# Kernel tuning notes

Hardware: AMD Instinct MI355X
Metric: run time of the kernel (lower is better)

Reference implementation:

```python
import jax, jax.numpy as jnp
import numpy as np

N, M, D = 100000, 5000, 2

def setup_inputs() -> dict:
    key = jax.random.key(0)
    k1, k2, k3 = jax.random.split(key, 3)
    euclidean_data = jax.random.normal(k1, (N, D), dtype=jnp.float32)
    maze_points = jax.random.normal(k2, (M, D), dtype=jnp.float32)
    ts_proj = jax.random.uniform(k3, (M,), dtype=jnp.float32)
    return {"euclidean_data": euclidean_data, "maze_points": maze_points, "ts_proj": ts_proj}

def reference(euclidean_data, maze_points, ts_proj):
    # squared distance matrix [N, M], reduced via argmin (1-NN)
    diff = euclidean_data[:, None, :] - maze_points[None, :, :]   # [N, M, D]
    dist2 = jnp.sum(jnp.square(diff), axis=-1)                    # [N, M]
    best = jnp.argmin(dist2, axis=1)                              # [N]
    projected_pos = maze_points[best]                             # [N, D]
    linear_pos = ts_proj[best]                                    # [N]
    return (projected_pos, linear_pos)
```

## Files before the change

### kernel.cpp

```cpp
#include <hip/hip_runtime.h>

#define N_Q  100000
#define N_M  5000
#define G    64
#define NC   (G * G)
#define RMAX 4
#define CS_OFF_B   64
#define SORT_OFF_B (CS_OFF_B + 16400)
#define OVF_OFF_B  (SORT_OFF_B + N_M * 16)
#define WS_NEED    (OVF_OFF_B + N_Q * 4)

__global__ __launch_bounds__(1024) void build_grid(
    const float* __restrict__ maze, const float* __restrict__ ts,
    float* __restrict__ ws)
{
    __shared__ float red[1024];
    __shared__ int   part[1024];
    __shared__ int   cnt[NC];
    const int t = threadIdx.x;
    if (t == 0) ((int*)ws)[8] = 0;

    float mnx = 1e30f, mxx = -1e30f, mny = 1e30f, mxy = -1e30f;
    for (int i = t; i < N_M; i += 1024) {
        const float x = maze[2 * i], y = maze[2 * i + 1];
        mnx = fminf(mnx, x); mxx = fmaxf(mxx, x);
        mny = fminf(mny, y); mxy = fmaxf(mxy, y);
    }
    auto reduce = [&](float v, bool domin) -> float {
        red[t] = v; __syncthreads();
        for (int s = 512; s > 0; s >>= 1) {
            if (t < s) {
                const float o = red[t + s];
                red[t] = domin ? fminf(red[t], o) : fmaxf(red[t], o);
            }
            __syncthreads();
        }
        const float r = red[0]; __syncthreads(); return r;
    };
    mnx = reduce(mnx, true);  mxx = reduce(mxx, false);
    mny = reduce(mny, true);  mxy = reduce(mxy, false);

    float cwx = (mxx - mnx) * (1.0f / G) * (1.0f + 1e-5f);
    float cwy = (mxy - mny) * (1.0f / G) * (1.0f + 1e-5f);
    if (!(cwx > 0.0f)) cwx = 1.0f;
    if (!(cwy > 0.0f)) cwy = 1.0f;
    const float ivx = 1.0f / cwx, ivy = 1.0f / cwy;
    if (t == 0) {
        ws[0] = mnx; ws[1] = mny; ws[2] = cwx;
        ws[3] = cwy; ws[4] = ivx; ws[5] = ivy;
    }

    for (int i = t; i < NC; i += 1024) cnt[i] = 0;
    __syncthreads();
    for (int i = t; i < N_M; i += 1024) {
        const float x = maze[2 * i], y = maze[2 * i + 1];
        const int cx = min(G - 1, max(0, (int)((x - mnx) * ivx)));
        const int cy = min(G - 1, max(0, (int)((y - mny) * ivy)));
        atomicAdd(&cnt[cy * G + cx], 1);
    }
    __syncthreads();

    int* cs = (int*)((char*)ws + CS_OFF_B);
    const int base = t * 4;
    int loc[4], sum = 0;
    #pragma unroll
    for (int j = 0; j < 4; ++j) { loc[j] = sum; sum += cnt[base + j]; }
    part[t] = sum; __syncthreads();
    for (int s = 1; s < 1024; s <<= 1) {
        const int v = (t >= s) ? part[t - s] : 0;
        __syncthreads();
        part[t] += v;
        __syncthreads();
    }
    const int excl = part[t] - sum;
    #pragma unroll
    for (int j = 0; j < 4; ++j) cs[base + j] = excl + loc[j];
    if (t == 0) cs[NC] = N_M;
    __syncthreads();
    #pragma unroll
    for (int j = 0; j < 4; ++j) cnt[base + j] = excl + loc[j];
    __syncthreads();

    float4* sorted = (float4*)((char*)ws + SORT_OFF_B);
    for (int i = t; i < N_M; i += 1024) {
        const float x = maze[2 * i], y = maze[2 * i + 1];
        const int cx = min(G - 1, max(0, (int)((x - mnx) * ivx)));
        const int cy = min(G - 1, max(0, (int)((y - mny) * ivy)));
        const int pos = atomicAdd(&cnt[cy * G + cx], 1);
        float4 e; e.x = x; e.y = y; e.z = ts[i]; e.w = __int_as_float(i);
        sorted[pos] = e;
    }
}

__global__ __launch_bounds__(256) void grid_query(
    const float* __restrict__ q, float* __restrict__ ws,
    float* __restrict__ out)
{
    const int qi = blockIdx.x * 256 + threadIdx.x;
    if (qi >= N_Q) return;

    const float mnx = ws[0], mny = ws[1], cwx = ws[2];
    const float cwy = ws[3], ivx = ws[4], ivy = ws[5];
    const int*    cs     = (const int*)((const char*)ws + CS_OFF_B);
    const float4* sorted = (const float4*)((const char*)ws + SORT_OFF_B);

    const float2 Q = ((const float2*)q)[qi];
    const float qx = Q.x, qy = Q.y;
    const int cx = min(G - 1, max(0, (int)((qx - mnx) * ivx)));
    const int cy = min(G - 1, max(0, (int)((qy - mny) * ivy)));

    float bd2 = 3.4e38f;
    int bidx = 0x7fffffff, bsp = 0;

    auto scan_pts = [&](int s, int e) {
        for (int p = s; p < e; ++p) {
            const float4 c = sorted[p];
            const float dx = __fsub_rn(qx, c.x);
            const float dy = __fsub_rn(qy, c.y);
            const float d2 = __fadd_rn(__fmul_rn(dx, dx), __fmul_rn(dy, dy));
            const int idx = __float_as_int(c.w);
            if (d2 < bd2 || (d2 == bd2 && idx < bidx)) { bd2 = d2; bidx = idx; bsp = p; }
        }
    };
    auto scan_row = [&](int rowbase, int xa, int xb) {
        int prev = cs[rowbase + xa];
        for (int x = xa; x <= xb; ++x) {
            const int nxt = cs[rowbase + x + 1];
            scan_pts(prev, nxt);
            prev = nxt;
        }
    };

    bool resolved = false;
    for (int r = 0; r <= RMAX; ++r) {
        const int x0 = max(0, cx - r), x1 = min(G - 1, cx + r);
        if (r == 0) {
            scan_row(cy * G, cx, cx);
        } else {
            if (cy - r >= 0)     scan_row((cy - r) * G, x0, x1);
            if (cy + r <= G - 1) scan_row((cy + r) * G, x0, x1);
            const int yy0 = max(0, cy - r + 1), yy1 = min(G - 1, cy + r - 1);
            if (cx - r >= 0)     for (int y = yy0; y <= yy1; ++y) { const int c0 = y * G + cx - r; scan_pts(cs[c0], cs[c0 + 1]); }
            if (cx + r <= G - 1) for (int y = yy0; y <= yy1; ++y) { const int c0 = y * G + cx + r; scan_pts(cs[c0], cs[c0 + 1]); }
        }
        const float Xlo = mnx + (float)(cx - r) * cwx;
        const float Xhi = mnx + (float)(cx + r + 1) * cwx;
        const float Ylo = mny + (float)(cy - r) * cwy;
        const float Yhi = mny + (float)(cy + r + 1) * cwy;
        float lb = fminf(fminf(qx - Xlo, Xhi - qx), fminf(qy - Ylo, Yhi - qy));
        lb = lb * 0.9999f - 1e-6f;
        if (lb > 0.0f && lb * lb > bd2) { resolved = true; break; }
    }

    if (resolved) {
        const float4 bw = sorted[bsp];
        out[2 * qi]       = bw.x;
        out[2 * qi + 1]   = bw.y;
        out[2 * N_Q + qi] = bw.z;
    } else {
        int* ovfc = (int*)ws + 8;
        const int pos = atomicAdd(ovfc, 1);
        ((int*)((char*)ws + OVF_OFF_B))[pos] = qi;
    }
}

__global__ __launch_bounds__(256) void brute_overflow(
    const float* __restrict__ q, const float* __restrict__ maze,
    const float* __restrict__ ts, const float* __restrict__ ws,
    float* __restrict__ out)
{
    const int cnt = ((const int*)ws)[8];
    const int* ovl = (const int*)((const char*)ws + OVF_OFF_B);
    const int wave  = (blockIdx.x * 256 + threadIdx.x) >> 6;
    const int lane  = threadIdx.x & 63;
    const int nwave = gridDim.x * 4;

    for (int w = wave; w < cnt; w += nwave) {
        const int qi = ovl[w];
        const float qx = q[2 * qi], qy = q[2 * qi + 1];
        float bd2 = 3.4e38f; int bidx = 0x7fffffff;
        for (int p = lane; p < N_M; p += 64) {
            const float2 c = ((const float2*)maze)[p];
            const float dx = __fsub_rn(qx, c.x);
            const float dy = __fsub_rn(qy, c.y);
            const float d2 = __fadd_rn(__fmul_rn(dx, dx), __fmul_rn(dy, dy));
            if (d2 < bd2 || (d2 == bd2 && p < bidx)) { bd2 = d2; bidx = p; }
        }
        #pragma unroll
        for (int s = 1; s < 64; s <<= 1) {
            const float ob = __shfl_xor(bd2, s);
            const int   oi = __shfl_xor(bidx, s);
            if (ob < bd2 || (ob == bd2 && oi < bidx)) { bd2 = ob; bidx = oi; }
        }
        if (lane == 0) {
            out[2 * qi]       = maze[2 * bidx];
            out[2 * qi + 1]   = maze[2 * bidx + 1];
            out[2 * N_Q + qi] = ts[bidx];
        }
    }
}

#define CW   4
#define CHK  1264
#define NPAD (CW * CHK)
#define FB_WS_BYTES (NPAD * 2 * 4)

typedef float v2f __attribute__((ext_vector_type(2)));
typedef float v8f __attribute__((ext_vector_type(8)));

__global__ void setup_soa(const float* __restrict__ maze, float* __restrict__ ws) {
    const int i = blockIdx.x * 256 + threadIdx.x;
    if (i >= NPAD) return;
    const int c = i / CHK, k = i - c * CHK;
    float x = 1e30f, y = 1e30f;
    const int g = c * 1250 + k;
    if (k < 1250) { x = -maze[2 * g]; y = -maze[2 * g + 1]; }
    ws[i] = x;
    ws[NPAD + i] = y;
}

#define LDX0(D) asm volatile("s_load_dwordx8 %0, %1, 0x0"    : "=s"(D) : "s"(xb))
#define LDX1(D) asm volatile("s_load_dwordx8 %0, %1, 0x20"   : "=s"(D) : "s"(xb))
#define LDY0(D) asm volatile("s_load_dwordx8 %0, %1, 0x4f00" : "=s"(D) : "s"(xb))
#define LDY1(D) asm volatile("s_load_dwordx8 %0, %1, 0x4f20" : "=s"(D) : "s"(xb))
#define WAIT4(a,b,c,d) asm volatile("s_waitcnt lgkmcnt(0)" : "+s"(a), "+s"(b), "+s"(c), "+s"(d))

#define PSTEP(X8, Y8, J) do {                                                 \
    v2f px_ = __builtin_shufflevector(X8, X8, 2*(J), 2*(J)+1);                \
    v2f py_ = __builtin_shufflevector(Y8, Y8, 2*(J), 2*(J)+1);                \
    v2f dx_, dy_;                                                             \
    asm("v_pk_add_f32 %0, %1, %2" : "=v"(dx_) : "s"(px_), "v"(qxx));          \
    asm("v_pk_add_f32 %0, %1, %2" : "=v"(dy_) : "s"(py_), "v"(qyy));          \
    asm("v_pk_mul_f32 %0, %0, %0" : "+v"(dx_));                               \
    asm("v_pk_mul_f32 %0, %0, %0" : "+v"(dy_));                               \
    asm("v_pk_add_f32 %0, %0, %1" : "+v"(dx_) : "v"(dy_));                    \
    float a_ = dx_.x, b_ = dx_.y;                                             \
    asm("v_min3_f32 %0, %1, %2, %0" : "+v"(bm) : "v"(a_), "v"(b_));           \
} while (0)

#define COMP(X0, X1, Y0, Y1, B) do {                                          \
    PSTEP(X0, Y0, 0); PSTEP(X0, Y0, 1); PSTEP(X0, Y0, 2); PSTEP(X0, Y0, 3);   \
    PSTEP(X1, Y1, 0); PSTEP(X1, Y1, 1); PSTEP(X1, Y1, 2); PSTEP(X1, Y1, 3);   \
    bb = (bm < prev) ? (B) : bb; prev = bm;                                   \
} while (0)

__global__ __launch_bounds__(256) void nn_scan(
    const float* __restrict__ q, const float* __restrict__ maze,
    const float* __restrict__ ts, const float* __restrict__ ws,
    float* __restrict__ out)
{
    __shared__ float sval[CW][64];
    __shared__ int   sidx[CW][64];
    const int lane = threadIdx.x & 63;
    const int wv   = __builtin_amdgcn_readfirstlane((int)(threadIdx.x >> 6));
    const int qi   = blockIdx.x * 64 + lane;
    const int qc   = qi < N_Q ? qi : N_Q - 1;
    const float2 Q = ((const float2*)q)[qc];
    const v2f qxx = { Q.x, Q.x };
    const v2f qyy = { Q.y, Q.y };
    unsigned long long xb = (unsigned long long)(const void*)(ws + (size_t)wv * CHK);
    v8f ax0, ax1, ay0, ay1, bx0, bx1, by0, by1;
    LDX0(ax0); LDX1(ax1); LDY0(ay0); LDY1(ay1); xb += 64;
    float bm = 3.4e38f, prev = 3.4e38f;
    int bb = 0;
    #pragma unroll 1
    for (int k = 0; k < 39; ++k) {
        WAIT4(ax0, ax1, ay0, ay1);
        LDX0(bx0); LDX1(bx1); LDY0(by0); LDY1(by1); xb += 64;
        COMP(ax0, ax1, ay0, ay1, 2 * k);
        WAIT4(bx0, bx1, by0, by1);
        LDX0(ax0); LDX1(ax1); LDY0(ay0); LDY1(ay1); xb += 64;
        COMP(bx0, bx1, by0, by1, 2 * k + 1);
    }
    WAIT4(ax0, ax1, ay0, ay1);
    COMP(ax0, ax1, ay0, ay1, 78);
    int fk = 0x7fffffff;
    {
        const float* xs = ws + (size_t)wv * CHK + (size_t)bb * 16;
        #pragma unroll
        for (int j = 0; j < 16; ++j) {
            const float dx = __fadd_rn(Q.x, xs[j]);
            const float dy = __fadd_rn(Q.y, xs[j + NPAD]);
            const float d2 = __fadd_rn(__fmul_rn(dx, dx), __fmul_rn(dy, dy));
            if (d2 == bm) fk = min(fk, bb * 16 + j);
        }
    }
    const int kloc = fk < 1250 ? fk : 1249;
    sval[wv][lane] = bm;
    sidx[wv][lane] = wv * 1250 + kloc;
    __syncthreads();
    if (wv == 0 && qi < N_Q) {
        float bv = sval[0][lane];
        int   bg = sidx[0][lane];
        #pragma unroll
        for (int c = 1; c < CW; ++c) {
            const float v = sval[c][lane];
            const int   g = sidx[c][lane];
            if (v < bv || (v == bv && g < bg)) { bv = v; bg = g; }
        }
        const float2 bp = ((const float2*)maze)[bg];
        out[2 * qi]       = bp.x;
        out[2 * qi + 1]   = bp.y;
        out[2 * N_Q + qi] = ts[bg];
    }
}

extern "C" void kernel_launch(void* const* d_in, const int* in_sizes, int n_in,
                              void* d_out, int out_size, void* d_ws, size_t ws_size,
                              hipStream_t stream) {
    const float* q    = (const float*)d_in[0];
    const float* maze = (const float*)d_in[1];
    const float* ts   = (const float*)d_in[2];
    float* out = (float*)d_out;

    if (ws_size >= (size_t)WS_NEED) {
        build_grid<<<1, 1024, 0, stream>>>(maze, ts, (float*)d_ws);
        grid_query<<<(N_Q + 255) / 256, 256, 0, stream>>>(q, (float*)d_ws, out);
        brute_overflow<<<256, 256, 0, stream>>>(q, maze, ts, (const float*)d_ws, out);
    } else {
        setup_soa<<<(NPAD + 255) / 256, 256, 0, stream>>>(maze, (float*)d_ws);
        nn_scan<<<(N_Q + 63) / 64, 256, 0, stream>>>(q, maze, ts,
                                                     (const float*)d_ws, out);
    }
}
```

Baseline: 76.81 us.

## Fuse overflow brute force into grid query and shrink grid search to two rings

The overflow kernel and its atomic queue are removed. Unresolved queries are now brute-forced inside the query kernel, with the whole wave cooperating on each unresolved lane found via ballot. The query scans the 3x3 neighborhood as three contiguous row ranges with 4-wide unrolled loads, then ring 2 only if needed, and falls back to brute force after that. The grid build uses 256 threads with wave-shuffle reductions instead of shared-memory tree reductions, saving a launch and barriers at the cost of divergence when some lanes need the fallback.

Measured after the change: 91.53 us. 1.19x slower.

```diff
diff --git a/kernel.cpp b/kernel.cpp
--- a/kernel.cpp
+++ b/kernel.cpp
@@ -4,55 +4,48 @@
 #define N_M  5000
 #define G    64
 #define NC   (G * G)
-#define RMAX 4
 #define CS_OFF_B   64
 #define SORT_OFF_B (CS_OFF_B + 16400)
-#define OVF_OFF_B  (SORT_OFF_B + N_M * 16)
-#define WS_NEED    (OVF_OFF_B + N_Q * 4)
-
-__global__ __launch_bounds__(1024) void build_grid(
+#define WS_NEED    (SORT_OFF_B + N_M * 16)
+
+__global__ __launch_bounds__(256) void build_grid(
     const float* __restrict__ maze, const float* __restrict__ ts,
     float* __restrict__ ws)
 {
-    __shared__ float red[1024];
-    __shared__ int   part[1024];
     __shared__ int   cnt[NC];
-    const int t = threadIdx.x;
-    if (t == 0) ((int*)ws)[8] = 0;
+    __shared__ int   part[256];
+    __shared__ float wred[4][4];
+    const int t = threadIdx.x, lane = t & 63, wv = t >> 6;
 
     float mnx = 1e30f, mxx = -1e30f, mny = 1e30f, mxy = -1e30f;
-    for (int i = t; i < N_M; i += 1024) {
+    for (int i = t; i < N_M; i += 256) {
         const float x = maze[2 * i], y = maze[2 * i + 1];
         mnx = fminf(mnx, x); mxx = fmaxf(mxx, x);
         mny = fminf(mny, y); mxy = fmaxf(mxy, y);
     }
-    auto reduce = [&](float v, bool domin) -> float {
-        red[t] = v; __syncthreads();
-        for (int s = 512; s > 0; s >>= 1) {
-            if (t < s) {
-                const float o = red[t + s];
-                red[t] = domin ? fminf(red[t], o) : fmaxf(red[t], o);
-            }
-            __syncthreads();
-        }
-        const float r = red[0]; __syncthreads(); return r;
-    };
-    mnx = reduce(mnx, true);  mxx = reduce(mxx, false);
-    mny = reduce(mny, true);  mxy = reduce(mxy, false);
+    #pragma unroll
+    for (int s = 1; s < 64; s <<= 1) {
+        mnx = fminf(mnx, __shfl_xor(mnx, s));
+        mxx = fmaxf(mxx, __shfl_xor(mxx, s));
+        mny = fminf(mny, __shfl_xor(mny, s));
+        mxy = fmaxf(mxy, __shfl_xor(mxy, s));
+    }
+    if (lane == 0) { wred[wv][0] = mnx; wred[wv][1] = mxx; wred[wv][2] = mny; wred[wv][3] = mxy; }
+    for (int i = t; i < NC; i += 256) cnt[i] = 0;
+    __syncthreads();
+    mnx = fminf(fminf(wred[0][0], wred[1][0]), fminf(wred[2][0], wred[3][0]));
+    mxx = fmaxf(fmaxf(wred[0][1], wred[1][1]), fmaxf(wred[2][1], wred[3][1]));
+    mny = fminf(fminf(wred[0][2], wred[1][2]), fminf(wred[2][2], wred[3][2]));
+    mxy = fmaxf(fmaxf(wred[0][3], wred[1][3]), fmaxf(wred[2][3], wred[3][3]));
 
     float cwx = (mxx - mnx) * (1.0f / G) * (1.0f + 1e-5f);
     float cwy = (mxy - mny) * (1.0f / G) * (1.0f + 1e-5f);
     if (!(cwx > 0.0f)) cwx = 1.0f;
     if (!(cwy > 0.0f)) cwy = 1.0f;
     const float ivx = 1.0f / cwx, ivy = 1.0f / cwy;
-    if (t == 0) {
-        ws[0] = mnx; ws[1] = mny; ws[2] = cwx;
-        ws[3] = cwy; ws[4] = ivx; ws[5] = ivy;
-    }
-
-    for (int i = t; i < NC; i += 1024) cnt[i] = 0;
-    __syncthreads();
-    for (int i = t; i < N_M; i += 1024) {
+    if (t == 0) { ws[0] = mnx; ws[1] = mny; ws[2] = cwx; ws[3] = cwy; ws[4] = ivx; ws[5] = ivy; }
+
+    for (int i = t; i < N_M; i += 256) {
         const float x = maze[2 * i], y = maze[2 * i + 1];
         const int cx = min(G - 1, max(0, (int)((x - mnx) * ivx)));
         const int cy = min(G - 1, max(0, (int)((y - mny) * ivy)));
@@ -61,12 +54,12 @@
     __syncthreads();
 
     int* cs = (int*)((char*)ws + CS_OFF_B);
-    const int base = t * 4;
-    int loc[4], sum = 0;
+    const int base = t * 16;
+    int loc[16], sum = 0;
     #pragma unroll
-    for (int j = 0; j < 4; ++j) { loc[j] = sum; sum += cnt[base + j]; }
+    for (int j = 0; j < 16; ++j) { loc[j] = sum; sum += cnt[base + j]; }
     part[t] = sum; __syncthreads();
-    for (int s = 1; s < 1024; s <<= 1) {
+    for (int s = 1; s < 256; s <<= 1) {
         const int v = (t >= s) ? part[t - s] : 0;
         __syncthreads();
         part[t] += v;
@@ -74,15 +67,15 @@
     }
     const int excl = part[t] - sum;
     #pragma unroll
-    for (int j = 0; j < 4; ++j) cs[base + j] = excl + loc[j];
+    for (int j = 0; j < 16; ++j) cs[base + j] = excl + loc[j];
     if (t == 0) cs[NC] = N_M;
     __syncthreads();
     #pragma unroll
-    for (int j = 0; j < 4; ++j) cnt[base + j] = excl + loc[j];
+    for (int j = 0; j < 16; ++j) cnt[base + j] = excl + loc[j];
     __syncthreads();
 
     float4* sorted = (float4*)((char*)ws + SORT_OFF_B);
-    for (int i = t; i < N_M; i += 1024) {
+    for (int i = t; i < N_M; i += 256) {
         const float x = maze[2 * i], y = maze[2 * i + 1];
         const int cx = min(G - 1, max(0, (int)((x - mnx) * ivx)));
         const int cy = min(G - 1, max(0, (int)((y - mny) * ivy)));
@@ -92,118 +85,109 @@
     }
 }
 
-__global__ __launch_bounds__(256) void grid_query(
-    const float* __restrict__ q, float* __restrict__ ws,
+__global__ __launch_bounds__(64) void grid_query(
+    const float* __restrict__ q, const float* __restrict__ maze,
+    const float* __restrict__ ts, const float* __restrict__ ws,
     float* __restrict__ out)
 {
-    const int qi = blockIdx.x * 256 + threadIdx.x;
-    if (qi >= N_Q) return;
+    const int lane = threadIdx.x;
+    const int qi = blockIdx.x * 64 + lane;
+    const int qc = qi < N_Q ? qi : N_Q - 1;
 
     const float mnx = ws[0], mny = ws[1], cwx = ws[2];
     const float cwy = ws[3], ivx = ws[4], ivy = ws[5];
     const int*    cs     = (const int*)((const char*)ws + CS_OFF_B);
     const float4* sorted = (const float4*)((const char*)ws + SORT_OFF_B);
 
-    const float2 Q = ((const float2*)q)[qi];
+    const float2 Q = ((const float2*)q)[qc];
     const float qx = Q.x, qy = Q.y;
     const int cx = min(G - 1, max(0, (int)((qx - mnx) * ivx)));
     const int cy = min(G - 1, max(0, (int)((qy - mny) * ivy)));
 
     float bd2 = 3.4e38f;
-    int bidx = 0x7fffffff, bsp = 0;
-
-    auto scan_pts = [&](int s, int e) {
-        for (int p = s; p < e; ++p) {
-            const float4 c = sorted[p];
-            const float dx = __fsub_rn(qx, c.x);
-            const float dy = __fsub_rn(qy, c.y);
-            const float d2 = __fadd_rn(__fmul_rn(dx, dx), __fmul_rn(dy, dy));
-            const int idx = __float_as_int(c.w);
-            if (d2 < bd2 || (d2 == bd2 && idx < bidx)) { bd2 = d2; bidx = idx; bsp = p; }
-        }
+    int bidx = 0x7fffffff;
+
+    auto cand = [&](const float4 c) {
+        const float dx = __fsub_rn(qx, c.x);
+        const float dy = __fsub_rn(qy, c.y);
+        const float d2 = __fadd_rn(__fmul_rn(dx, dx), __fmul_rn(dy, dy));
+        const int idx = __float_as_int(c.w);
+        if (d2 < bd2 || (d2 == bd2 && idx < bidx)) { bd2 = d2; bidx = idx; }
     };
-    auto scan_row = [&](int rowbase, int xa, int xb) {
-        int prev = cs[rowbase + xa];
-        for (int x = xa; x <= xb; ++x) {
-            const int nxt = cs[rowbase + x + 1];
-            scan_pts(prev, nxt);
-            prev = nxt;
+    auto scan4 = [&](int s, int e) {
+        for (int p = s; p < e; p += 4) {
+            const float4 c0 = sorted[p];
+            const float4 c1 = sorted[p + 1 < e ? p + 1 : p];
+            const float4 c2 = sorted[p + 2 < e ? p + 2 : p];
+            const float4 c3 = sorted[p + 3 < e ? p + 3 : p];
+            cand(c0); cand(c1); cand(c2); cand(c3);
         }
     };
-
-    bool resolved = false;
-    for (int r = 0; r <= RMAX; ++r) {
-        const int x0 = max(0, cx - r), x1 = min(G - 1, cx + r);
-        if (r == 0) {
-            scan_row(cy * G, cx, cx);
-        } else {
-            if (cy - r >= 0)     scan_row((cy - r) * G, x0, x1);
-            if (cy + r <= G - 1) scan_row((cy + r) * G, x0, x1);
-            const int yy0 = max(0, cy - r + 1), yy1 = min(G - 1, cy + r - 1);
-            if (cx - r >= 0)     for (int y = yy0; y <= yy1; ++y) { const int c0 = y * G + cx - r; scan_pts(cs[c0], cs[c0 + 1]); }
-            if (cx + r <= G - 1) for (int y = yy0; y <= yy1; ++y) { const int c0 = y * G + cx + r; scan_pts(cs[c0], cs[c0 + 1]); }
-        }
+    auto bound_ok = [&](int r) -> bool {
         const float Xlo = mnx + (float)(cx - r) * cwx;
         const float Xhi = mnx + (float)(cx + r + 1) * cwx;
         const float Ylo = mny + (float)(cy - r) * cwy;
         const float Yhi = mny + (float)(cy + r + 1) * cwy;
         float lb = fminf(fminf(qx - Xlo, Xhi - qx), fminf(qy - Ylo, Yhi - qy));
         lb = lb * 0.9999f - 1e-6f;
-        if (lb > 0.0f && lb * lb > bd2) { resolved = true; break; }
-    }
-
-    if (resolved) {
-        const float4 bw = sorted[bsp];
-        out[2 * qi]       = bw.x;
-        out[2 * qi + 1]   = bw.y;
-        out[2 * N_Q + qi] = bw.z;
-    } else {
-        int* ovfc = (int*)ws + 8;
-        const int pos = atomicAdd(ovfc, 1);
-        ((int*)((char*)ws + OVF_OFF_B))[pos] = qi;
-    }
-}
-
-__global__ __launch_bounds__(256) void brute_overflow(
-    const float* __restrict__ q, const float* __restrict__ maze,
-    const float* __restrict__ ts, const float* __restrict__ ws,
-    float* __restrict__ out)
-{
-    const int cnt = ((const int*)ws)[8];
-    const int* ovl = (const int*)((const char*)ws + OVF_OFF_B);
-    const int wave  = (blockIdx.x * 256 + threadIdx.x) >> 6;
-    const int lane  = threadIdx.x & 63;
-    const int nwave = gridDim.x * 4;
-
-    for (int w = wave; w < cnt; w += nwave) {
-        const int qi = ovl[w];
-        const float qx = q[2 * qi], qy = q[2 * qi + 1];
-        float bd2 = 3.4e38f; int bidx = 0x7fffffff;
+        return (lb > 0.0f) && (lb * lb > bd2);
+    };
+
+    {
+        const int x0 = max(0, cx - 1), x1 = min(G - 1, cx + 1);
+        const int rA = max(0, cy - 1) * G, rB = cy * G, rC = min(G - 1, cy + 1) * G;
+        const int sA = cs[rA + x0], eA = cs[rA + x1 + 1];
+        const int sB = cs[rB + x0], eB = cs[rB + x1 + 1];
+        const int sC = cs[rC + x0], eC = cs[rC + x1 + 1];
+        scan4(sA, eA); scan4(sB, eB); scan4(sC, eC);
+    }
+    bool resolved = bound_ok(1);
+
+    if (__any(!resolved)) {
+        if (!resolved) {
+            const int X0 = max(0, cx - 2), X1 = min(G - 1, cx + 2);
+            if (cy - 2 >= 0)     { const int rb = (cy - 2) * G; scan4(cs[rb + X0], cs[rb + X1 + 1]); }
+            if (cy + 2 <= G - 1) { const int rb = (cy + 2) * G; scan4(cs[rb + X0], cs[rb + X1 + 1]); }
+            const int Y0 = max(0, cy - 1), Y1 = min(G - 1, cy + 1);
+            if (cx - 2 >= 0)     for (int y = Y0; y <= Y1; ++y) { const int c0 = y * G + cx - 2; scan4(cs[c0], cs[c0 + 1]); }
+            if (cx + 2 <= G - 1) for (int y = Y0; y <= Y1; ++y) { const int c0 = y * G + cx + 2; scan4(cs[c0], cs[c0 + 1]); }
+            resolved = bound_ok(2);
+        }
+    }
+
+    unsigned long long mask = __ballot(!resolved);
+    while (mask) {
+        const int l = __ffsll((unsigned long long)mask) - 1;
+        mask &= mask - 1;
+        const float bx = __shfl(qx, l), by = __shfl(qy, l);
+        float vb = 3.4e38f; int vi = 0x7fffffff;
+        #pragma unroll 4
         for (int p = lane; p < N_M; p += 64) {
             const float2 c = ((const float2*)maze)[p];
-            const float dx = __fsub_rn(qx, c.x);
-            const float dy = __fsub_rn(qy, c.y);
+            const float dx = __fsub_rn(bx, c.x);
+            const float dy = __fsub_rn(by, c.y);
             const float d2 = __fadd_rn(__fmul_rn(dx, dx), __fmul_rn(dy, dy));
-            if (d2 < bd2 || (d2 == bd2 && p < bidx)) { bd2 = d2; bidx = p; }
+            if (d2 < vb || (d2 == vb && p < vi)) { vb = d2; vi = p; }
         }
         #pragma unroll
         for (int s = 1; s < 64; s <<= 1) {
-            const float ob = __shfl_xor(bd2, s);
-            const int   oi = __shfl_xor(bidx, s);
-            if (ob < bd2 || (ob == bd2 && oi < bidx)) { bd2 = ob; bidx = oi; }
-        }
-        if (lane == 0) {
-            out[2 * qi]       = maze[2 * bidx];
-            out[2 * qi + 1]   = maze[2 * bidx + 1];
-            out[2 * N_Q + qi] = ts[bidx];
-        }
+            const float ob = __shfl_xor(vb, s);
+            const int   oi = __shfl_xor(vi, s);
+            if (ob < vb || (ob == vb && oi < vi)) { vb = ob; vi = oi; }
+        }
+        if (lane == l) { bd2 = vb; bidx = (vi < N_M ? vi : N_M - 1); }
+    }
+
+    if (qi < N_Q) {
+        out[2 * qi]       = maze[2 * bidx];
+        out[2 * qi + 1]   = maze[2 * bidx + 1];
+        out[2 * N_Q + qi] = ts[bidx];
     }
 }
 
 #define CW   4
 #define CHK  1264
 #define NPAD (CW * CHK)
-#define FB_WS_BYTES (NPAD * 2 * 4)
 
 typedef float v2f __attribute__((ext_vector_type(2)));
 typedef float v8f __attribute__((ext_vector_type(8)));
@@ -314,9 +298,9 @@
     float* out = (float*)d_out;
 
     if (ws_size >= (size_t)WS_NEED) {
-        build_grid<<<1, 1024, 0, stream>>>(maze, ts, (float*)d_ws);
-        grid_query<<<(N_Q + 255) / 256, 256, 0, stream>>>(q, (float*)d_ws, out);
-        brute_overflow<<<256, 256, 0, stream>>>(q, maze, ts, (const float*)d_ws, out);
+        build_grid<<<1, 256, 0, stream>>>(maze, ts, (float*)d_ws);
+        grid_query<<<(N_Q + 63) / 64, 64, 0, stream>>>(q, maze, ts,
+                                                       (const float*)d_ws, out);
     } else {
         setup_soa<<<(NPAD + 255) / 256, 256, 0, stream>>>(maze, (float*)d_ws);
         nn_scan<<<(N_Q + 63) / 64, 256, 0, stream>>>(q, maze, ts,
```

## Batch candidate loads and merge 3x3 neighborhood rows into contiguous scans

Applied to the files above, without the earlier changes.

The grid query now scans the initial 3x3 cell block as three contiguous row ranges instead of walking rings 0 and 1 cell by cell. Points are loaded in unrolled groups of 8 or 4, with clamped indices, so several memory loads are in flight at once. Outer rings are entered only while some lane in the wave is unresolved. The winner is fetched from maze and ts by index rather than through a stored sorted position. Duplicate clamped loads do redundant compute, and this saves no work when cells hold few points.

After: 73.65 us. 1.04x faster.

```diff
diff --git a/kernel.cpp b/kernel.cpp
--- a/kernel.cpp
+++ b/kernel.cpp
@@ -93,7 +93,8 @@
 }
 
 __global__ __launch_bounds__(256) void grid_query(
-    const float* __restrict__ q, float* __restrict__ ws,
+    const float* __restrict__ q, const float* __restrict__ maze,
+    const float* __restrict__ ts, float* __restrict__ ws,
     float* __restrict__ out)
 {
     const int qi = blockIdx.x * 256 + threadIdx.x;
@@ -110,53 +111,74 @@
     const int cy = min(G - 1, max(0, (int)((qy - mny) * ivy)));
 
     float bd2 = 3.4e38f;
-    int bidx = 0x7fffffff, bsp = 0;
-
-    auto scan_pts = [&](int s, int e) {
-        for (int p = s; p < e; ++p) {
-            const float4 c = sorted[p];
-            const float dx = __fsub_rn(qx, c.x);
-            const float dy = __fsub_rn(qy, c.y);
-            const float d2 = __fadd_rn(__fmul_rn(dx, dx), __fmul_rn(dy, dy));
-            const int idx = __float_as_int(c.w);
-            if (d2 < bd2 || (d2 == bd2 && idx < bidx)) { bd2 = d2; bidx = idx; bsp = p; }
-        }
-    };
-    auto scan_row = [&](int rowbase, int xa, int xb) {
-        int prev = cs[rowbase + xa];
-        for (int x = xa; x <= xb; ++x) {
-            const int nxt = cs[rowbase + x + 1];
-            scan_pts(prev, nxt);
-            prev = nxt;
-        }
-    };
-
-    bool resolved = false;
-    for (int r = 0; r <= RMAX; ++r) {
-        const int x0 = max(0, cx - r), x1 = min(G - 1, cx + r);
-        if (r == 0) {
-            scan_row(cy * G, cx, cx);
-        } else {
-            if (cy - r >= 0)     scan_row((cy - r) * G, x0, x1);
-            if (cy + r <= G - 1) scan_row((cy + r) * G, x0, x1);
-            const int yy0 = max(0, cy - r + 1), yy1 = min(G - 1, cy + r - 1);
-            if (cx - r >= 0)     for (int y = yy0; y <= yy1; ++y) { const int c0 = y * G + cx - r; scan_pts(cs[c0], cs[c0 + 1]); }
-            if (cx + r <= G - 1) for (int y = yy0; y <= yy1; ++y) { const int c0 = y * G + cx + r; scan_pts(cs[c0], cs[c0 + 1]); }
-        }
+    int bidx = 0x7fffffff;
+
+    auto cand = [&](const float4 c) {
+        const float dx = __fsub_rn(qx, c.x);
+        const float dy = __fsub_rn(qy, c.y);
+        const float d2 = __fadd_rn(__fmul_rn(dx, dx), __fmul_rn(dy, dy));
+        const int idx = __float_as_int(c.w);
+        if (d2 < bd2 || (d2 == bd2 && idx < bidx)) { bd2 = d2; bidx = idx; }
+    };
+    auto scan8 = [&](int s, int e) {
+        for (int p = s; p < e; p += 8) {
+            const float4 c0 = sorted[p];
+            const float4 c1 = sorted[p + 1 < e ? p + 1 : p];
+            const float4 c2 = sorted[p + 2 < e ? p + 2 : p];
+            const float4 c3 = sorted[p + 3 < e ? p + 3 : p];
+            const float4 c4 = sorted[p + 4 < e ? p + 4 : p];
+            const float4 c5 = sorted[p + 5 < e ? p + 5 : p];
+            const float4 c6 = sorted[p + 6 < e ? p + 6 : p];
+            const float4 c7 = sorted[p + 7 < e ? p + 7 : p];
+            cand(c0); cand(c1); cand(c2); cand(c3);
+            cand(c4); cand(c5); cand(c6); cand(c7);
+        }
+    };
+    auto scan4 = [&](int s, int e) {
+        for (int p = s; p < e; p += 4) {
+            const float4 c0 = sorted[p];
+            const float4 c1 = sorted[p + 1 < e ? p + 1 : p];
+            const float4 c2 = sorted[p + 2 < e ? p + 2 : p];
+            const float4 c3 = sorted[p + 3 < e ? p + 3 : p];
+            cand(c0); cand(c1); cand(c2); cand(c3);
+        }
+    };
+    auto bound_ok = [&](int r) -> bool {
         const float Xlo = mnx + (float)(cx - r) * cwx;
         const float Xhi = mnx + (float)(cx + r + 1) * cwx;
         const float Ylo = mny + (float)(cy - r) * cwy;
         const float Yhi = mny + (float)(cy + r + 1) * cwy;
         float lb = fminf(fminf(qx - Xlo, Xhi - qx), fminf(qy - Ylo, Yhi - qy));
         lb = lb * 0.9999f - 1e-6f;
-        if (lb > 0.0f && lb * lb > bd2) { resolved = true; break; }
+        return (lb > 0.0f) && (lb * lb > bd2);
+    };
+
+    {
+        const int x0 = max(0, cx - 1), x1 = min(G - 1, cx + 1);
+        const int rA = max(0, cy - 1) * G, rB = cy * G, rC = min(G - 1, cy + 1) * G;
+        const int sA = cs[rA + x0], eA = cs[rA + x1 + 1];
+        const int sB = cs[rB + x0], eB = cs[rB + x1 + 1];
+        const int sC = cs[rC + x0], eC = cs[rC + x1 + 1];
+        scan8(sA, eA); scan8(sB, eB); scan8(sC, eC);
+    }
+    bool resolved = bound_ok(1);
+
+    for (int r = 2; r <= RMAX && __any(!resolved); ++r) {
+        if (!resolved) {
+            const int X0 = max(0, cx - r), X1 = min(G - 1, cx + r);
+            if (cy - r >= 0)     { const int rb = (cy - r) * G; scan8(cs[rb + X0], cs[rb + X1 + 1]); }
+            if (cy + r <= G - 1) { const int rb = (cy + r) * G; scan8(cs[rb + X0], cs[rb + X1 + 1]); }
+            const int Y0 = max(0, cy - r + 1), Y1 = min(G - 1, cy + r - 1);
+            if (cx - r >= 0)     for (int y = Y0; y <= Y1; ++y) { const int c0 = y * G + cx - r; scan4(cs[c0], cs[c0 + 1]); }
+            if (cx + r <= G - 1) for (int y = Y0; y <= Y1; ++y) { const int c0 = y * G + cx + r; scan4(cs[c0], cs[c0 + 1]); }
+            resolved = bound_ok(r);
+        }
     }
 
     if (resolved) {
-        const float4 bw = sorted[bsp];
-        out[2 * qi]       = bw.x;
-        out[2 * qi + 1]   = bw.y;
-        out[2 * N_Q + qi] = bw.z;
+        out[2 * qi]       = maze[2 * bidx];
+        out[2 * qi + 1]   = maze[2 * bidx + 1];
+        out[2 * N_Q + qi] = ts[bidx];
     } else {
         int* ovfc = (int*)ws + 8;
         const int pos = atomicAdd(ovfc, 1);
@@ -203,7 +225,6 @@
 #define CW   4
 #define CHK  1264
 #define NPAD (CW * CHK)
-#define FB_WS_BYTES (NPAD * 2 * 4)
 
 typedef float v2f __attribute__((ext_vector_type(2)));
 typedef float v8f __attribute__((ext_vector_type(8)));
@@ -315,7 +336,8 @@
 
     if (ws_size >= (size_t)WS_NEED) {
         build_grid<<<1, 1024, 0, stream>>>(maze, ts, (float*)d_ws);
-        grid_query<<<(N_Q + 255) / 256, 256, 0, stream>>>(q, (float*)d_ws, out);
+        grid_query<<<(N_Q + 255) / 256, 256, 0, stream>>>(q, maze, ts,
+                                                          (float*)d_ws, out);
         brute_overflow<<<256, 256, 0, stream>>>(q, maze, ts, (const float*)d_ws, out);
     } else {
         setup_soa<<<(NPAD + 255) / 256, 256, 0, stream>>>(maze, (float*)d_ws);
```
